# Optimization experiments

Measured on AMD Instinct MI355X. Metric: run time of the kernel, lower is better.

Reference implementation:

```python
import jax, jax.numpy as jnp
import numpy as np

P, K, D = 512, 4, 256          # identities, instances per id per modality, feature dim
N = 2 * P * K                  # two modality halves, as assumed by mod_idxs in the module
R_STRENGTH = 2.0               # cmrr_loss __init__ r=2.0 (soft_rank regularization_strength)


def _soft_rank_kl(values, reg_strength):
    """torchsort.soft_rank(values, regularization='kl', strength=reg_strength), rows of length n.

    theta = values/strength; sort descending -> s; w = [n,...,1].
    isotonic_kl solves argmin_{v noninc} <e^{s-v},1> + <w, v>; block value on [i..j] is
    LSE(s[i:j+1]) - LSE(log w[i:j+1]). Min-max formula (valid for PAV-solvable problems):
      dual_k = min_{i<=k} max_{j>=k} B[i,j].
    ranks = exp(s - dual) scattered back by the inverse permutation.
    """
    n = values.shape[1]
    theta = values * (1.0 / reg_strength)
    perm = jnp.argsort(-theta, axis=1)                     # descending sort order
    s = jnp.take_along_axis(theta, perm, axis=1)
    inv_perm = jnp.argsort(perm, axis=1)
    logw = jnp.log(jnp.arange(n, 0, -1, dtype=values.dtype))  # log([n, n-1, ..., 1])
    k = jnp.arange(n)
    ii, jj, kk = k[:, None, None], k[None, :, None], k[None, None, :]
    # segment [i, max(i,j)]; for invalid i>j it degenerates to {i} so LSE stays finite (no NaN grads)
    seg = (kk >= ii) & (kk <= jnp.maximum(jj, ii))         # (n, n, n) indexed [i, j, k]
    neg = jnp.asarray(-jnp.inf, values.dtype)
    lse_s = jax.nn.logsumexp(jnp.where(seg[None], s[:, None, None, :], neg), axis=-1)  # (R,n,n)
    lse_w = jax.nn.logsumexp(jnp.where(seg, logw[None, None, :], neg), axis=-1)        # (n,n)
    valid = k[:, None] <= k[None, :]                       # i <= j
    B = jnp.where(valid[None], lse_s - lse_w[None], neg)   # block values, -inf where invalid
    T = jax.lax.cummax(B, axis=2, reverse=True)            # T[:,i,k] = max_{j>=k} B[:,i,j]
    tri = k[:, None] <= k[None, :]                         # i <= k
    dual = jnp.min(jnp.where(tri[None], T, jnp.inf), axis=1)  # (R, n), nonincreasing
    return jnp.exp(jnp.take_along_axis(s - dual, inv_perm, axis=1))


def _pairwise_dist(f):
    # ||f_i - f_j||_2 with clamp(min=1e-12) before sqrt, as in the module
    sq = jnp.sum(f * f, axis=1)
    d2 = sq[:, None] + sq[None, :] - 2.0 * (f @ f.T)
    return jnp.sqrt(jnp.clip(d2, 1e-12, None))


def _spearman(a, b):
    a = a - jnp.mean(a, axis=1, keepdims=True)
    a = a / jnp.linalg.norm(a, axis=1, keepdims=True)
    b = b - jnp.mean(b, axis=1, keepdims=True)
    b = b / jnp.linalg.norm(b, axis=1, keepdims=True)
    return jnp.sum(a * b, axis=1)


def setup_inputs() -> dict:
    key = jax.random.key(0)
    k0, k1, k2 = jax.random.split(key, 3)
    ids = jnp.repeat(jnp.arange(P), K)                     # PK sampling within each modality
    target = jnp.concatenate([ids, ids])                   # first half modality 0, second half modality 1
    f0 = jax.random.normal(k0, (N, D), jnp.float32)
    f1 = jax.random.normal(k1, (N, D), jnp.float32)
    f2 = jax.random.normal(k2, (N, D), jnp.float32)
    return {"f0": f0, "f1": f1, "f2": f2, "target": target, "k_pos": K}


def reference(f0, f1, f2, target, k_pos):
    feats = (f0, f1, f2)
    n = target.shape[0]
    pos = target[None, :] == target[:, None]
    mod = jnp.concatenate([jnp.zeros(n // 2, jnp.int32), jnp.ones(n // 2, jnp.int32)])
    mask = pos & (mod[None, :] != mod[:, None])            # pos_idxs & ~mod_idxs
    # boolean-mask gather dists[mask].view(N,-1): per row, the k_pos True columns in increasing order
    idx = jnp.argsort(jnp.where(mask, 0, 1), axis=1, stable=True)[:, :k_pos]
    ranks = []
    for f in feats:
        dists = _pairwise_dist(f)
        dist_intra = jnp.take_along_axis(dists, idx, axis=1)   # (N, k_pos)
        ranks.append(_soft_rank_kl(dist_intra, R_STRENGTH))
    L = len(feats)
    loss = jnp.zeros((n,), f0.dtype)
    for i in range(L):
        for j in range(i + 1, L):
            loss = loss + (_spearman(ranks[i], ranks[j]) + 1.0) / 2.0
    loss = loss / (L * (L - 1) / 2.0)
    return jnp.mean(loss)
```

## Files before the change

kernel.cpp:

```cpp
#include <hip/hip_runtime.h>
#include <hip/hip_bf16.h>


__device__ __forceinline__ void soft_rank4(const float d2[4], float r[4]) {
    float th[4]; int p[4] = {0, 1, 2, 3};
#pragma unroll
    for (int t = 0; t < 4; ++t) th[t] = 0.5f * sqrtf(fmaxf(d2[t], 1e-12f));
#define CSWAP(a, b)                                                           \
    if (th[a] < th[b]) {                                                      \
        float tt = th[a]; th[a] = th[b]; th[b] = tt;                          \
        int tp = p[a]; p[a] = p[b]; p[b] = tp;                                \
    }
    CSWAP(0, 1) CSWAP(1, 2) CSWAP(2, 3) CSWAP(0, 1) CSWAP(1, 2) CSWAP(0, 1)
#undef CSWAP
    const float logW[4][4] = {
        {1.3862944f, 1.9459101f, 2.1972246f, 2.3025851f},
        {0.f,        1.0986123f, 1.6094379f, 1.7917595f},
        {0.f,        0.f,        0.6931472f, 1.0986123f},
        {0.f,        0.f,        0.f,        0.f}};
    float B[4][4];
#pragma unroll
    for (int i = 0; i < 4; ++i) {
        float run = 0.f;
#pragma unroll
        for (int j = 0; j < 4; ++j) {
            if (j >= i) {
                run += __expf(th[j] - th[i]);
                B[i][j] = th[i] + __logf(run) - logW[i][j];
            }
        }
    }
    float rs[4];
#pragma unroll
    for (int k = 0; k < 4; ++k) {
        float dual = 1e30f;
#pragma unroll
        for (int i = 0; i < 4; ++i) {
            if (i <= k) {
                float mx = -1e30f;
#pragma unroll
                for (int j = 0; j < 4; ++j)
                    if (j >= k) mx = fmaxf(mx, B[i][j]);
                dual = fminf(dual, mx);
            }
        }
        rs[k] = __expf(th[k] - dual);
    }
#pragma unroll
    for (int t = 0; t < 4; ++t) {
        float v = rs[3];
        v = (p[2] == t) ? rs[2] : v;
        v = (p[1] == t) ? rs[1] : v;
        v = (p[0] == t) ? rs[0] : v;
        r[t] = v;
    }
}

__device__ __forceinline__ float spearman4(const float a[4], const float b[4]) {
    float ma = 0.25f * (a[0] + a[1] + a[2] + a[3]);
    float mb = 0.25f * (b[0] + b[1] + b[2] + b[3]);
    float sab = 0.f, saa = 0.f, sbb = 0.f;
#pragma unroll
    for (int t = 0; t < 4; ++t) {
        float x = a[t] - ma, y = b[t] - mb;
        sab += x * y; saa += x * x; sbb += y * y;
    }
    return sab * rsqrtf(saa * sbb);
}

__device__ __forceinline__ float row_loss(const float d2a[3][4]) {
    float ranks[3][4];
#pragma unroll
    for (int f = 0; f < 3; ++f) soft_rank4(d2a[f], ranks[f]);
    const float c01 = spearman4(ranks[0], ranks[1]);
    const float c02 = spearman4(ranks[0], ranks[2]);
    const float c12 = spearman4(ranks[1], ranks[2]);
    return (c01 + c02 + c12 + 3.f) * (0.5f / 3.f);
}

__global__ __launch_bounds__(256) void cmrr_fused(
        const float* __restrict__ f0, const float* __restrict__ f1,
        const float* __restrict__ f2, const int* __restrict__ target,
        float* __restrict__ ws, float* __restrict__ out, int N, float inv_n,
        int nblocks) {
    const float* F[3] = {f0, f1, f2};
    const int g = blockIdx.x;
    const int wave = threadIdx.x >> 6;
    const int lane = threadIdx.x & 63;
    const int half = N >> 1;

    __shared__ float4 stage[256];
    __shared__ float d2s[3][4][4];
    __shared__ float lsum[4];

    const int r0 = 4 * g + wave;
    const int id = target[4 * g];
    const int jbase = half + 4 * id;

#pragma unroll
    for (int f = 0; f < 3; ++f) {
        if (f) __syncthreads();
        stage[threadIdx.x] =
            ((const float4*)(F[f] + (size_t)jbase * 256))[threadIdx.x];
        __syncthreads();
        const float4 a = ((const float4*)(F[f] + (size_t)r0 * 256))[lane];
        float d2[4];
#pragma unroll
        for (int j = 0; j < 4; ++j) {
            const float4 b = stage[j * 64 + lane];
            const float dx = a.x - b.x, dy = a.y - b.y;
            const float dz = a.z - b.z, dw = a.w - b.w;
            float v = dx * dx + dy * dy + dz * dz + dw * dw;
#pragma unroll
            for (int m = 32; m >= 1; m >>= 1) v += __shfl_xor(v, m, 64);
            d2[j] = v;
        }
        if (lane == 0) {
#pragma unroll
            for (int j = 0; j < 4; ++j) d2s[f][wave][j] = d2[j];
        }
    }
    __syncthreads();

    float d2a[3][4], d2b[3][4];
#pragma unroll
    for (int f = 0; f < 3; ++f) {
#pragma unroll
        for (int t = 0; t < 4; ++t) {
            d2a[f][t] = d2s[f][wave][t];
            d2b[f][t] = d2s[f][t][wave];
        }
    }
    const float loss2 = row_loss(d2a) + row_loss(d2b);
    if (lane == 0) lsum[wave] = loss2;
    __syncthreads();

    if (threadIdx.x == 0) {
        const float partial = (lsum[0] + lsum[1]) + (lsum[2] + lsum[3]);
        atomicAdd(ws, partial);
        __threadfence();
        unsigned old = atomicAdd((unsigned*)(ws + 1), 1u);
        if (old == (unsigned)(nblocks - 1)) {
            const float total = atomicAdd(ws, 0.0f);
            out[0] = total * inv_n;
        }
    }
}

extern "C" void kernel_launch(void* const* d_in, const int* in_sizes, int n_in,
                              void* d_out, int out_size, void* d_ws,
                              size_t ws_size, hipStream_t stream) {
    const float* f0 = (const float*)d_in[0];
    const float* f1 = (const float*)d_in[1];
    const float* f2 = (const float*)d_in[2];
    const int* target = (const int*)d_in[3];
    const int N = in_sizes[3];
    const int nblocks = N / 8;
    hipMemsetAsync(d_ws, 0, 16, stream);
    cmrr_fused<<<nblocks, 256, 0, stream>>>(f0, f1, f2, target, (float*)d_ws,
                                            (float*)d_out, N, 1.0f / (float)N,
                                            nblocks);
}
```

Before: 87.70 us.

## Compute each 4x4 block with a single wave using a transposed butterfly reduction

Each block now runs as one 64-lane wave instead of four waves. The wave loads all 4 anchor rows and 4 partner rows for the three feature sets into registers, so the shared-memory staging and __syncthreads are gone. The 48 partial squared distances are reduced together with a recursive-halving transposed shuffle reduction, which needs far fewer shuffles than 48 separate butterflies. The reduced distances are then redistributed by shuffle to 8 lanes that each compute one row or column loss. The cost is much higher register pressure (a 64-float array plus 24 float4 loads), and each block now has a quarter as many threads.

```diff
diff --git a/kernel.cpp b/kernel.cpp
--- a/kernel.cpp
+++ b/kernel.cpp
@@ -78,68 +78,85 @@
     return (c01 + c02 + c12 + 3.f) * (0.5f / 3.f);
 }
 
-__global__ __launch_bounds__(256) void cmrr_fused(
+__global__ __launch_bounds__(64) void cmrr_fused(
         const float* __restrict__ f0, const float* __restrict__ f1,
         const float* __restrict__ f2, const int* __restrict__ target,
         float* __restrict__ ws, float* __restrict__ out, int N, float inv_n,
         int nblocks) {
     const float* F[3] = {f0, f1, f2};
     const int g = blockIdx.x;
-    const int wave = threadIdx.x >> 6;
-    const int lane = threadIdx.x & 63;
+    const int lane = threadIdx.x;
     const int half = N >> 1;
-
-    __shared__ float4 stage[256];
-    __shared__ float d2s[3][4][4];
-    __shared__ float lsum[4];
-
-    const int r0 = 4 * g + wave;
     const int id = target[4 * g];
     const int jbase = half + 4 * id;
 
+    float4 A[3][4], Bv[3][4];
 #pragma unroll
     for (int f = 0; f < 3; ++f) {
-        if (f) __syncthreads();
-        stage[threadIdx.x] =
-            ((const float4*)(F[f] + (size_t)jbase * 256))[threadIdx.x];
-        __syncthreads();
-        const float4 a = ((const float4*)(F[f] + (size_t)r0 * 256))[lane];
-        float d2[4];
+        const float4* pa = (const float4*)(F[f] + (size_t)(4 * g) * 256);
 #pragma unroll
-        for (int j = 0; j < 4; ++j) {
-            const float4 b = stage[j * 64 + lane];
-            const float dx = a.x - b.x, dy = a.y - b.y;
-            const float dz = a.z - b.z, dw = a.w - b.w;
-            float v = dx * dx + dy * dy + dz * dz + dw * dw;
+        for (int i = 0; i < 4; ++i) A[f][i] = pa[i * 64 + lane];
+    }
 #pragma unroll
-            for (int m = 32; m >= 1; m >>= 1) v += __shfl_xor(v, m, 64);
-            d2[j] = v;
-        }
-        if (lane == 0) {
+    for (int f = 0; f < 3; ++f) {
+        const float4* pb = (const float4*)(F[f] + (size_t)jbase * 256);
 #pragma unroll
-            for (int j = 0; j < 4; ++j) d2s[f][wave][j] = d2[j];
+        for (int j = 0; j < 4; ++j) Bv[f][j] = pb[j * 64 + lane];
+    }
+
+    float c[64];
+#pragma unroll
+    for (int f = 0; f < 3; ++f) {
+#pragma unroll
+        for (int i = 0; i < 4; ++i) {
+#pragma unroll
+            for (int j = 0; j < 4; ++j) {
+                const float4 a = A[f][i], b = Bv[f][j];
+                const float dx = a.x - b.x, dy = a.y - b.y;
+                const float dz = a.z - b.z, dw = a.w - b.w;
+                c[f * 16 + i * 4 + j] = dx * dx + dy * dy + dz * dz + dw * dw;
+            }
         }
     }
-    __syncthreads();
+#pragma unroll
+    for (int v = 48; v < 64; ++v) c[v] = 0.f;
 
-    float d2a[3][4], d2b[3][4];
+#pragma unroll
+    for (int s = 0; s < 6; ++s) {
+        const int bit = 1 << s;
+        const bool hi = (lane & bit) != 0;
+#pragma unroll
+        for (int k = 0; k < 32; ++k) {
+            if (k < (32 >> s)) {
+                const float lo_v = c[2 * k], hi_v = c[2 * k + 1];
+                const float send = hi ? lo_v : hi_v;
+                const float recv = __shfl_xor(send, bit, 64);
+                c[k] = (hi ? hi_v : lo_v) + recv;
+            }
+        }
+    }
+    const float red = c[0];
+
+    const int r = lane & 7;
+    const bool isRow = r < 4;
+    float d2[3][4];
 #pragma unroll
     for (int f = 0; f < 3; ++f) {
 #pragma unroll
         for (int t = 0; t < 4; ++t) {
-            d2a[f][t] = d2s[f][wave][t];
-            d2b[f][t] = d2s[f][t][wave];
+            const int src = f * 16 + (isRow ? (r * 4 + t) : (t * 4 + (r - 4)));
+            d2[f][t] = __shfl(red, src, 64);
         }
     }
-    const float loss2 = row_loss(d2a) + row_loss(d2b);
-    if (lane == 0) lsum[wave] = loss2;
-    __syncthreads();
+    float loss = row_loss(d2);
+    loss = (lane < 8) ? loss : 0.f;
+#pragma unroll
+    for (int m = 32; m >= 1; m >>= 1) loss += __shfl_xor(loss, m, 64);
 
-    if (threadIdx.x == 0) {
-        const float partial = (lsum[0] + lsum[1]) + (lsum[2] + lsum[3]);
-        atomicAdd(ws, partial);
+    if (lane == 0) {
+        atomicAdd(ws, loss);
         __threadfence();
-        unsigned old = atomicAdd((unsigned*)(ws + 1), 1u);
+        const unsigned old = atomicAdd((unsigned*)(ws + 1), 1u);
         if (old == (unsigned)(nblocks - 1)) {
             const float total = atomicAdd(ws, 0.0f);
             out[0] = total * inv_n;
@@ -157,7 +174,7 @@
     const int N = in_sizes[3];
     const int nblocks = N / 8;
     hipMemsetAsync(d_ws, 0, 16, stream);
-    cmrr_fused<<<nblocks, 256, 0, stream>>>(f0, f1, f2, target, (float*)d_ws,
-                                            (float*)d_out, N, 1.0f / (float)N,
-                                            nblocks);
+    cmrr_fused<<<nblocks, 64, 0, stream>>>(f0, f1, f2, target, (float*)d_ws,
+                                           (float*)d_out, N, 1.0f / (float)N,
+                                           nblocks);
 }
```

After: 86.05 us. Within noise of the previous version (-1.9%).
